# Optimization experiments

Hardware: AMD Instinct MI355X
Metric: run time of the kernel (lower is better)

## Reference

```python
import jax, jax.numpy as jnp
import numpy as np

NUM_ITERATIONS = 3


def _squash(t, axis=-1):
    sq = jnp.sum(t * t, axis=axis, keepdims=True)
    return (sq / (1.0 + sq)) * t / jnp.sqrt(sq)


def setup_inputs() -> dict:
    key = jax.random.key(0)
    k1, k2 = jax.random.split(key)
    B, R, CIN = 256, 1152, 8
    NCAPS, COUT = 10, 16
    x = jax.random.normal(k1, (B, R, CIN), dtype=jnp.float32)
    route_weights = jax.random.normal(k2, (NCAPS, R, CIN, COUT), dtype=jnp.float32)
    return {"x": x, "route_weights": route_weights}


def reference(x, route_weights):
    # priors: [caps, B, route, 1, out] == x[None,:,:,None,:] @ W[:,None,:,:,:]
    priors = jnp.einsum('bri,crio->cbro', x, route_weights)[:, :, :, None, :]
    logits = jnp.zeros_like(priors)  # [caps, B, route, 1, out]
    outputs = None
    for i in range(NUM_ITERATIONS):
        probs = jax.nn.softmax(logits, axis=2)  # softmax over route nodes
        outputs = _squash(jnp.sum(probs * priors, axis=2, keepdims=True))
        if i != NUM_ITERATIONS - 1:
            logits = logits + jnp.sum(priors * outputs, axis=-1, keepdims=True)
    return outputs  # [caps, B, 1, 1, out]
```

## Files before the change

kernel.cpp:

```cpp
#include <hip/hip_runtime.h>
#include <cstddef>

#define NCAPS  10
#define BATCH  256
#define NROUTE 1152
#define CIN    8
#define COUT   16
#define T      1024
#define NB     2
#define NWAVE  (T / 64)
#define NBLK   (NCAPS * (BATCH / NB))
#define PLANE  (NROUTE * 8)
#define XPLANE (NROUTE * CIN)

__device__ __forceinline__ unsigned swzu(unsigned unit) { return unit ^ ((unit >> 3) & 3u); }

__device__ __forceinline__ unsigned pack_bf16(float a, float b) {
    unsigned ua = __float_as_uint(a); ua += 0x7fffu + ((ua >> 16) & 1u);
    unsigned ub = __float_as_uint(b); ub += 0x7fffu + ((ub >> 16) & 1u);
    return (ua >> 16) | (ub & 0xffff0000u);
}
__device__ __forceinline__ float blo(unsigned u) { return __uint_as_float(u << 16); }
__device__ __forceinline__ float bhi(unsigned u) { return __uint_as_float(u & 0xffff0000u); }

__device__ __forceinline__ float wave_sum(float v) {
    v += __shfl_xor(v, 1);  v += __shfl_xor(v, 2);  v += __shfl_xor(v, 4);
    v += __shfl_xor(v, 8);  v += __shfl_xor(v, 16); v += __shfl_xor(v, 32);
    return v;
}

__device__ __forceinline__ float wave_sum16(float* s, int lane) {
#pragma unroll
    for (int j = 0; j < 8; ++j) {
        float snd = (lane & 1) ? s[j] : s[j + 8];
        float r = __shfl_xor(snd, 1);
        s[j] = ((lane & 1) ? s[j + 8] : s[j]) + r;
    }
#pragma unroll
    for (int j = 0; j < 4; ++j) {
        float snd = (lane & 2) ? s[j] : s[j + 4];
        float r = __shfl_xor(snd, 2);
        s[j] = ((lane & 2) ? s[j + 4] : s[j]) + r;
    }
#pragma unroll
    for (int j = 0; j < 2; ++j) {
        float snd = (lane & 4) ? s[j] : s[j + 2];
        float r = __shfl_xor(snd, 4);
        s[j] = ((lane & 4) ? s[j + 2] : s[j]) + r;
    }
    {
        float snd = (lane & 8) ? s[0] : s[1];
        float r = __shfl_xor(snd, 8);
        s[0] = ((lane & 8) ? s[1] : s[0]) + r;
    }
    s[0] += __shfl_xor(s[0], 16);
    s[0] += __shfl_xor(s[0], 32);
    return s[0];
}

union U4 { uint4 v; unsigned u[4]; };
union U2 { uint2 v; unsigned u[2]; };

__device__ __forceinline__ void phaseA_unit(int u, const float* __restrict__ Wc,
                                            const float* __restrict__ xb,
                                            unsigned* prLDS) {
    const int r  = u >> 2;
    const int j4 = u & 3;
    float xs[NB][CIN];
#pragma unroll
    for (int b = 0; b < NB; ++b) {
        const float4* xq = (const float4*)(xb + (size_t)b * XPLANE + r * CIN);
        float4 xa = xq[0], xv = xq[1];
        xs[b][0] = xa.x; xs[b][1] = xa.y; xs[b][2] = xa.z; xs[b][3] = xa.w;
        xs[b][4] = xv.x; xs[b][5] = xv.y; xs[b][6] = xv.z; xs[b][7] = xv.w;
    }
    float4 acc[NB];
#pragma unroll
    for (int b = 0; b < NB; ++b) acc[b] = make_float4(0.f, 0.f, 0.f, 0.f);
    const float* wq = Wc + (size_t)r * (CIN * COUT) + j4 * 4;
#pragma unroll
    for (int i = 0; i < CIN; ++i) {
        float4 w = *(const float4*)(wq + i * COUT);
#pragma unroll
        for (int b = 0; b < NB; ++b) {
            acc[b].x = fmaf(xs[b][i], w.x, acc[b].x);
            acc[b].y = fmaf(xs[b][i], w.y, acc[b].y);
            acc[b].z = fmaf(xs[b][i], w.z, acc[b].z);
            acc[b].w = fmaf(xs[b][i], w.w, acc[b].w);
        }
    }
    const unsigned base = swzu(2u * (unsigned)r + (unsigned)(j4 >> 1)) * 4u
                        + (unsigned)(j4 & 1) * 2u;
#pragma unroll
    for (int b = 0; b < NB; ++b) {
        U2 q;
        q.u[0] = pack_bf16(acc[b].x, acc[b].y);
        q.u[1] = pack_bf16(acc[b].z, acc[b].w);
        *(uint2*)&prLDS[b * PLANE + base] = q.v;
    }
}

__global__ __launch_bounds__(T) void caps_routing(const float* __restrict__ x,
                                                  const float* __restrict__ W,
                                                  float* __restrict__ out) {
    __shared__ unsigned prLDS[NB * PLANE];
    __shared__ float sred[NWAVE][20];
    __shared__ __align__(16) float VLDS[NB][COUT];

    const int tid  = threadIdx.x;
    const int lane = tid & 63;
    const int wv   = tid >> 6;

    int g    = blockIdx.x;
    int widx = (g & 7) * (NBLK / 8) + (g >> 3);
    int c    = widx >> 7;
    int b0   = (widx & 127) * NB;

    const float* Wc = W + (size_t)c * (NROUTE * CIN * COUT);
    const float* xb = x + (size_t)b0 * XPLANE;

#pragma unroll 1
    for (int pass = 0; pass < 4; ++pass) {
        phaseA_unit(pass * T + tid, Wc, xb, prLDS);
    }
    if (tid < 512) {
        phaseA_unit(4 * T + tid, Wc, xb, prLDS);
    }
    __syncthreads();

    const int bb = tid >> 9;
    const int tl = tid & 511;
    const int r2 = 1024 + (tl >> 2);
    const int j2 = tl & 3;
    const int comp = ((lane & 1) << 3) | ((lane & 2) << 1) | ((lane & 4) >> 1) | ((lane & 8) >> 3);

#pragma unroll 1
    for (int it = 0; it < 3; ++it) {
        float s16[COUT];
        float se = 0.f;
#pragma unroll
        for (int o = 0; o < COUT; ++o) s16[o] = 0.f;

#pragma unroll
        for (int k = 0; k < 2; ++k) {
            const int r = (k << 9) + tl;
            const unsigned d0 = bb * PLANE + swzu(2u * (unsigned)r) * 4u;
            const unsigned d1 = bb * PLANE + swzu(2u * (unsigned)r + 1u) * 4u;
            U4 qa, qb;
            qa.v = *(const uint4*)&prLDS[d0];
            qb.v = *(const uint4*)&prLDS[d1];
            float p[COUT];
#pragma unroll
            for (int q = 0; q < 4; ++q) {
                p[2 * q]     = blo(qa.u[q]);  p[2 * q + 1] = bhi(qa.u[q]);
                p[8 + 2 * q] = blo(qb.u[q]);  p[9 + 2 * q] = bhi(qb.u[q]);
            }
            float e;
            if (it > 0) {
                float d = 0.f;
#pragma unroll
                for (int q = 0; q < 4; ++q) {
                    float4 v4 = *(const float4*)&VLDS[bb][4 * q];
                    d = fmaf(p[4 * q + 0], v4.x, d);
                    d = fmaf(p[4 * q + 1], v4.y, d);
                    d = fmaf(p[4 * q + 2], v4.z, d);
                    d = fmaf(p[4 * q + 3], v4.w, d);
                }
                e = __expf(d);
            } else {
                e = 1.f;
            }
            se += e;
#pragma unroll
            for (int o = 0; o < COUT; ++o) s16[o] = fmaf(e, p[o], s16[o]);
        }

        {
            const unsigned dw = bb * PLANE + swzu(2u * (unsigned)r2 + (unsigned)(j2 >> 1)) * 4u
                              + (unsigned)(j2 & 1) * 2u;
            U2 q;
            q.v = *(const uint2*)&prLDS[dw];
            float pl[4] = {blo(q.u[0]), bhi(q.u[0]), blo(q.u[1]), bhi(q.u[1])};
            float e2;
            if (it > 0) {
                float d2 = 0.f;
#pragma unroll
                for (int j = 0; j < 4; ++j) d2 = fmaf(pl[j], VLDS[bb][4 * j2 + j], d2);
                d2 += __shfl_xor(d2, 1);
                d2 += __shfl_xor(d2, 2);
                e2 = __expf(d2);
            } else {
                e2 = 1.f;
            }
            se += 0.25f * e2;
#pragma unroll
            for (int o = 0; o < COUT; ++o) {
                const float add = e2 * pl[o & 3];
                s16[o] += ((o >> 2) == j2) ? add : 0.f;
            }
        }

        const float sv  = wave_sum16(s16, lane);
        const float sev = wave_sum(se);
        if (lane < 16) sred[wv][comp] = sv;
        if (lane == 0) sred[wv][16]   = sev;
        __syncthreads();

        if (tid < NB * COUT) {
            const int b = tid >> 4, o = tid & 15;
            float S = 0.f, SE = 0.f;
#pragma unroll
            for (int w = 0; w < 8; ++w) {
                S  += sred[b * 8 + w][o];
                SE += sred[b * 8 + w][16];
            }
            const float tt = S / SE;
            float pq = tt * tt;
            pq += __shfl_xor(pq, 1); pq += __shfl_xor(pq, 2);
            pq += __shfl_xor(pq, 4); pq += __shfl_xor(pq, 8);
            const float scale = pq / ((1.f + pq) * sqrtf(pq));
            const float val = tt * scale;
            if (it == 2) {
                out[((size_t)c * BATCH + b0 + b) * COUT + o] = val;
            } else {
                VLDS[b][o] = (it == 0) ? val : (VLDS[b][o] + val);
            }
        }
        __syncthreads();
    }
}

extern "C" void kernel_launch(void* const* d_in, const int* in_sizes, int n_in,
                              void* d_out, int out_size, void* d_ws, size_t ws_size,
                              hipStream_t stream) {
    const float* x = (const float*)d_in[0];
    const float* w = (const float*)d_in[1];
    float* out = (float*)d_out;
    hipLaunchKernelGGL(caps_routing, dim3(NBLK), dim3(T), 0, stream, x, w, out);
}
```

Measured before the change: 75.83 us.

## Run routing iterations in one wave per batch item, removing block syncs

Restructures the routing phase so a single wave per batch element iterates over all routes with software-prefetched LDS reads, keeping the output vector in registers and reducing via wave shuffles. This removes the cross-wave shared-memory reduction and block-wide barriers per iteration. In exchange, most waves of the block sit idle during routing and each active wave does several times more serial work. Also adds a min-blocks hint to the launch bounds.

Measured after the change: 131.5 us. 1.73x slower.

```diff
diff --git a/kernel.cpp b/kernel.cpp
--- a/kernel.cpp
+++ b/kernel.cpp
@@ -100,12 +100,10 @@
     }
 }
 
-__global__ __launch_bounds__(T) void caps_routing(const float* __restrict__ x,
-                                                  const float* __restrict__ W,
-                                                  float* __restrict__ out) {
+__global__ __launch_bounds__(T, 8) void caps_routing(const float* __restrict__ x,
+                                                     const float* __restrict__ W,
+                                                     float* __restrict__ out) {
     __shared__ unsigned prLDS[NB * PLANE];
-    __shared__ float sred[NWAVE][20];
-    __shared__ __align__(16) float VLDS[NB][COUT];
 
     const int tid  = threadIdx.x;
     const int lane = tid & 63;
@@ -128,105 +126,81 @@
     }
     __syncthreads();
 
-    const int bb = tid >> 9;
-    const int tl = tid & 511;
-    const int r2 = 1024 + (tl >> 2);
-    const int j2 = tl & 3;
-    const int comp = ((lane & 1) << 3) | ((lane & 2) << 1) | ((lane & 4) >> 1) | ((lane & 8) >> 3);
+    if (wv < NB) {
+        const int b = wv;
+        const unsigned pbase = (unsigned)b * PLANE;
+        const int comp = ((lane & 1) << 3) | ((lane & 2) << 1) | ((lane & 4) >> 1) | ((lane & 8) >> 3);
+
+        float V[COUT];
+#pragma unroll
+        for (int j = 0; j < COUT; ++j) V[j] = 0.f;
 
 #pragma unroll 1
-    for (int it = 0; it < 3; ++it) {
-        float s16[COUT];
-        float se = 0.f;
-#pragma unroll
-        for (int o = 0; o < COUT; ++o) s16[o] = 0.f;
-
-#pragma unroll
-        for (int k = 0; k < 2; ++k) {
-            const int r = (k << 9) + tl;
-            const unsigned d0 = bb * PLANE + swzu(2u * (unsigned)r) * 4u;
-            const unsigned d1 = bb * PLANE + swzu(2u * (unsigned)r + 1u) * 4u;
+        for (int it = 0; it < 3; ++it) {
+            float s16[COUT];
+#pragma unroll
+            for (int o = 0; o < COUT; ++o) s16[o] = 0.f;
+            float se = 0.f;
+
             U4 qa, qb;
-            qa.v = *(const uint4*)&prLDS[d0];
-            qb.v = *(const uint4*)&prLDS[d1];
-            float p[COUT];
-#pragma unroll
-            for (int q = 0; q < 4; ++q) {
-                p[2 * q]     = blo(qa.u[q]);  p[2 * q + 1] = bhi(qa.u[q]);
-                p[8 + 2 * q] = blo(qb.u[q]);  p[9 + 2 * q] = bhi(qb.u[q]);
+            {
+                const unsigned u0 = 2u * (unsigned)lane;
+                qa.v = *(const uint4*)&prLDS[pbase + swzu(u0) * 4u];
+                qb.v = *(const uint4*)&prLDS[pbase + swzu(u0 + 1u) * 4u];
             }
-            float e;
-            if (it > 0) {
-                float d = 0.f;
+#pragma unroll 1
+            for (int k = 0; k < 18; ++k) {
+                U4 na, nb;
+                if (k < 17) {
+                    const unsigned un = 2u * (unsigned)((k + 1) * 64 + lane);
+                    na.v = *(const uint4*)&prLDS[pbase + swzu(un) * 4u];
+                    nb.v = *(const uint4*)&prLDS[pbase + swzu(un + 1u) * 4u];
+                }
+                float e;
+                if (it > 0) {
+                    float d0 = 0.f, d1 = 0.f;
+#pragma unroll
+                    for (int q = 0; q < 4; ++q) {
+                        d0 = fmaf(blo(qa.u[q]), V[2 * q],     d0);
+                        d1 = fmaf(bhi(qa.u[q]), V[2 * q + 1], d1);
+                        d0 = fmaf(blo(qb.u[q]), V[8 + 2 * q], d0);
+                        d1 = fmaf(bhi(qb.u[q]), V[9 + 2 * q], d1);
+                    }
+                    e = __expf(d0 + d1);
+                } else {
+                    e = 1.f;
+                }
+                se += e;
 #pragma unroll
                 for (int q = 0; q < 4; ++q) {
-                    float4 v4 = *(const float4*)&VLDS[bb][4 * q];
-                    d = fmaf(p[4 * q + 0], v4.x, d);
-                    d = fmaf(p[4 * q + 1], v4.y, d);
-                    d = fmaf(p[4 * q + 2], v4.z, d);
-                    d = fmaf(p[4 * q + 3], v4.w, d);
-                }
-                e = __expf(d);
-            } else {
-                e = 1.f;
+                    s16[2 * q]     = fmaf(e, blo(qa.u[q]), s16[2 * q]);
+                    s16[2 * q + 1] = fmaf(e, bhi(qa.u[q]), s16[2 * q + 1]);
+                    s16[8 + 2 * q] = fmaf(e, blo(qb.u[q]), s16[8 + 2 * q]);
+                    s16[9 + 2 * q] = fmaf(e, bhi(qb.u[q]), s16[9 + 2 * q]);
+                }
+                qa = na; qb = nb;
             }
-            se += e;
-#pragma unroll
-            for (int o = 0; o < COUT; ++o) s16[o] = fmaf(e, p[o], s16[o]);
-        }
-
-        {
-            const unsigned dw = bb * PLANE + swzu(2u * (unsigned)r2 + (unsigned)(j2 >> 1)) * 4u
-                              + (unsigned)(j2 & 1) * 2u;
-            U2 q;
-            q.v = *(const uint2*)&prLDS[dw];
-            float pl[4] = {blo(q.u[0]), bhi(q.u[0]), blo(q.u[1]), bhi(q.u[1])};
-            float e2;
-            if (it > 0) {
-                float d2 = 0.f;
-#pragma unroll
-                for (int j = 0; j < 4; ++j) d2 = fmaf(pl[j], VLDS[bb][4 * j2 + j], d2);
-                d2 += __shfl_xor(d2, 1);
-                d2 += __shfl_xor(d2, 2);
-                e2 = __expf(d2);
-            } else {
-                e2 = 1.f;
-            }
-            se += 0.25f * e2;
-#pragma unroll
-            for (int o = 0; o < COUT; ++o) {
-                const float add = e2 * pl[o & 3];
-                s16[o] += ((o >> 2) == j2) ? add : 0.f;
-            }
-        }
-
-        const float sv  = wave_sum16(s16, lane);
-        const float sev = wave_sum(se);
-        if (lane < 16) sred[wv][comp] = sv;
-        if (lane == 0) sred[wv][16]   = sev;
-        __syncthreads();
-
-        if (tid < NB * COUT) {
-            const int b = tid >> 4, o = tid & 15;
-            float S = 0.f, SE = 0.f;
-#pragma unroll
-            for (int w = 0; w < 8; ++w) {
-                S  += sred[b * 8 + w][o];
-                SE += sred[b * 8 + w][16];
-            }
+
+            const float S  = wave_sum16(s16, lane);
+            const float SE = wave_sum(se);
             const float tt = S / SE;
             float pq = tt * tt;
             pq += __shfl_xor(pq, 1); pq += __shfl_xor(pq, 2);
             pq += __shfl_xor(pq, 4); pq += __shfl_xor(pq, 8);
             const float scale = pq / ((1.f + pq) * sqrtf(pq));
             const float val = tt * scale;
+
             if (it == 2) {
-                out[((size_t)c * BATCH + b0 + b) * COUT + o] = val;
+                if (lane < 16)
+                    out[((size_t)c * BATCH + b0 + b) * COUT + comp] = val;
             } else {
-                VLDS[b][o] = (it == 0) ? val : (VLDS[b][o] + val);
+#pragma unroll
+                for (int j = 0; j < COUT; ++j) {
+                    const int src = ((j & 1) << 3) | ((j & 2) << 1) | ((j & 4) >> 1) | ((j & 8) >> 3);
+                    V[j] += __shfl(val, src);
+                }
             }
         }
-        __syncthreads();
     }
 }
 
```
